# Kernel optimization log

Measured on AMD Instinct MI355X. Metric: run time of the kernel, lower is better.

## Reference

```python
import jax, jax.numpy as jnp
import numpy as np

KERNEL_MUL = 2.0
KERNEL_NUM = 5


def setup_inputs() -> dict:
    key = jax.random.key(0)
    k1, k2 = jax.random.split(key)
    source_features = jax.random.normal(k1, (4096, 1024), dtype=jnp.float32)
    target_features = jax.random.normal(k2, (4096, 1024), dtype=jnp.float32)
    return {"source_features": source_features, "target_features": target_features}


def reference(source_features, target_features):
    n = source_features.shape[0]
    total = jnp.concatenate([source_features, target_features], axis=0)  # [L, D]
    L = total.shape[0]
    # Pairwise squared distances via gram trick (same math as sum((a-b)**2)).
    sq = jnp.sum(total * total, axis=1)  # [L]
    d2 = jnp.maximum(sq[:, None] + sq[None, :] - 2.0 * (total @ total.T), 0.0)  # [L, L]
    # Median-heuristic-style bandwidth: mean of off-diagonal distances.
    bandwidth = jnp.sum(d2) / (L * L - L)
    bandwidth = bandwidth / (KERNEL_MUL ** (KERNEL_NUM // 2))
    # Multi-bandwidth RBF kernel sum (fixed small loop over KERNEL_NUM).
    kernel = jnp.zeros_like(d2)
    for i in range(KERNEL_NUM):
        kernel = kernel + jnp.exp(-d2 / (bandwidth * (KERNEL_MUL ** i)))
    kernel = kernel / KERNEL_NUM
    ss = jnp.mean(kernel[:n, :n])
    tt = jnp.mean(kernel[n:, n:])
    st = jnp.mean(kernel[:n, n:])
    return ss + tt - 2.0 * st
```

## Files before the change

kernel.cpp:

```cpp
#include <hip/hip_runtime.h>
#include <hip/hip_bf16.h>
#include <stdint.h>


#define L_TOTAL 8192
#define D_FEAT  1024
#define N_HALF  4096
#define TILE    128
#define TTILES  64
#define NBLK    (TTILES*(TTILES+1)/2)
#define BK      64

typedef __bf16 bf16_t;
typedef __bf16 bf16x4_t __attribute__((ext_vector_type(4)));
typedef __bf16 bf16x8_t __attribute__((ext_vector_type(8)));
typedef float  f32x4_t  __attribute__((ext_vector_type(4)));

#define XB_OFF   0
#define SQ_OFF   (L_TOTAL * D_FEAT * 2)
#define COL_OFF  (SQ_OFF + L_TOTAL * 4)
#define SACC_OFF (COL_OFF + D_FEAT * 4)
#define C1_OFF   (SACC_OFF + 8)

__device__ __forceinline__ void async_ld16(void* lds, const void* g) {
  auto ldsp = (__attribute__((address_space(3))) void*)(uintptr_t)lds;
  auto gp   = (const __attribute__((address_space(1))) void*)(uintptr_t)g;
  __builtin_amdgcn_global_load_lds(gp, ldsp, 16, 0, 0);
}

extern "C" __global__ __launch_bounds__(256) void k_zero(
    float* __restrict__ colsum, double* __restrict__ S_acc)
{
  const int tid = threadIdx.x;
  for (int c = tid; c < D_FEAT; c += 256) colsum[c] = 0.f;
  if (tid == 0) *S_acc = 0.0;
}

extern "C" __global__ __launch_bounds__(256) void k_prep(
    const float* __restrict__ src, const float* __restrict__ tgt,
    bf16_t* __restrict__ Xb, float* __restrict__ sq, float* __restrict__ colsum)
{
  __shared__ float cs[4][D_FEAT];
  const int tid  = threadIdx.x;
  const int lane = tid & 63;
  const int w    = tid >> 6;
  const int rbase = blockIdx.x * 32 + w * 8;

  float csp[16];
  #pragma unroll
  for (int j = 0; j < 16; ++j) csp[j] = 0.f;

  for (int i = 0; i < 8; ++i) {
    const int row = rbase + i;
    const float* xr = (row < N_HALF) ? (src + (size_t)row * D_FEAT)
                                     : (tgt + (size_t)(row - N_HALF) * D_FEAT);
    float s = 0.f;
    #pragma unroll
    for (int q = 0; q < 4; ++q) {
      const float4 v = ((const float4*)xr)[q * 64 + lane];
      bf16x4_t bv;
      bv[0] = (bf16_t)v.x; bv[1] = (bf16_t)v.y; bv[2] = (bf16_t)v.z; bv[3] = (bf16_t)v.w;
      *(bf16x4_t*)(Xb + (size_t)row * D_FEAT + (q * 64 + lane) * 4) = bv;
      const float g0 = (float)bv[0], g1 = (float)bv[1], g2 = (float)bv[2], g3 = (float)bv[3];
      s += g0 * g0 + g1 * g1 + g2 * g2 + g3 * g3;
      csp[q * 4 + 0] += v.x; csp[q * 4 + 1] += v.y;
      csp[q * 4 + 2] += v.z; csp[q * 4 + 3] += v.w;
    }
    #pragma unroll
    for (int off = 32; off > 0; off >>= 1) s += __shfl_down(s, off);
    if (lane == 0) sq[row] = s;
  }

  #pragma unroll
  for (int q = 0; q < 4; ++q) {
    float4 v4 = make_float4(csp[q*4+0], csp[q*4+1], csp[q*4+2], csp[q*4+3]);
    *(float4*)&cs[w][(q * 64 + lane) * 4] = v4;
  }
  __syncthreads();
  #pragma unroll
  for (int k = 0; k < 4; ++k) {
    const int c = tid * 4 + k;
    atomicAdd(&colsum[c], cs[0][c] + cs[1][c] + cs[2][c] + cs[3][c]);
  }
}

extern "C" __global__ __launch_bounds__(1024) void k_bw(
    const float* __restrict__ sq, const float* __restrict__ colsum,
    float* __restrict__ c1out)
{
  const int tid = threadIdx.x;
  double t = 0.0;
  for (int i = tid; i < L_TOTAL; i += 1024) t += (double)sq[i];
  t *= 2.0 * (double)L_TOTAL;
  if (tid < D_FEAT) { double v = colsum[tid]; t -= 2.0 * v * v; }
  __shared__ double red[1024];
  red[tid] = t;
  __syncthreads();
  for (int off = 512; off > 0; off >>= 1) {
    if (tid < off) red[tid] += red[tid + off];
    __syncthreads();
  }
  if (tid == 0) {
    double bw = red[0] / ((double)L_TOTAL * (double)L_TOTAL - (double)L_TOTAL);
    bw = bw / 4.0;
    *c1out = (float)(-1.4426950408889634 / (16.0 * bw));
  }
}

extern "C" __global__ __launch_bounds__(256) void k_mmd(
    const bf16_t* __restrict__ Xb, const float* __restrict__ sq,
    const float* __restrict__ c1ptr, double* __restrict__ S_acc)
{
  __shared__ __align__(16) char smem[2 * TILE * BK * 2];
  bf16_t* As = (bf16_t*)smem;
  bf16_t* Bs = (bf16_t*)(smem + TILE * BK * 2);

  const int b = (blockIdx.x & 7) * (NBLK / 8) + (blockIdx.x >> 3);
  int ti = (int)((sqrtf(8.f * (float)b + 1.f) - 1.f) * 0.5f);
  while ((ti + 1) * (ti + 2) / 2 <= b) ++ti;
  while (ti * (ti + 1) / 2 > b) --ti;
  const int tj = b - ti * (ti + 1) / 2;
  const int row0 = ti * TILE, col0 = tj * TILE;

  const int tid  = threadIdx.x;
  const int lane = tid & 63;
  const int w    = tid >> 6;
  const int wr   = w >> 1, wc = w & 1;

  const int srow = lane >> 3;
  const int scol = ((lane & 7) ^ srow) * 8;
  uint32_t offA[4], offB[4];
  #pragma unroll
  for (int q = 0; q < 4; ++q) {
    const int ch = w * 4 + q;
    offA[q] = (uint32_t)(row0 + ch * 8 + srow) * D_FEAT + scol;
    offB[q] = (uint32_t)(col0 + ch * 8 + srow) * D_FEAT + scol;
  }

  const int x = lane >> 4, y = lane & 7, rlo = lane & 15;
  const int baA0 = (wr * 64 + rlo) * (BK * 2) + ((x ^ y) * 16);
  const int baB0 = (wc * 64 + rlo) * (BK * 2) + ((x ^ y) * 16);
  const int baA1 = baA0 ^ 64;
  const int baB1 = baB0 ^ 64;
  const char* Ac = (const char*)As;
  const char* Bc = (const char*)Bs;

  f32x4_t acc[4][4] = {};

  for (int k0 = 0; k0 < D_FEAT; k0 += BK) {
    #pragma unroll
    for (int q = 0; q < 4; ++q) {
      async_ld16(&As[(w * 4 + q) * 512], Xb + offA[q] + k0);
      async_ld16(&Bs[(w * 4 + q) * 512], Xb + offB[q] + k0);
    }
    __syncthreads();

    bf16x8_t af0[4], af1[4], bf0[4], bf1[4];
    #pragma unroll
    for (int m = 0; m < 4; ++m) {
      af0[m] = *(const bf16x8_t*)(Ac + baA0 + m * 2048);
      af1[m] = *(const bf16x8_t*)(Ac + baA1 + m * 2048);
    }
    #pragma unroll
    for (int n = 0; n < 4; ++n) {
      bf0[n] = *(const bf16x8_t*)(Bc + baB0 + n * 2048);
      bf1[n] = *(const bf16x8_t*)(Bc + baB1 + n * 2048);
    }
    #pragma unroll
    for (int m = 0; m < 4; ++m)
      #pragma unroll
      for (int n = 0; n < 4; ++n)
        acc[m][n] = __builtin_amdgcn_mfma_f32_16x16x32_bf16(af0[m], bf0[n], acc[m][n], 0, 0, 0);
    #pragma unroll
    for (int m = 0; m < 4; ++m)
      #pragma unroll
      for (int n = 0; n < 4; ++n)
        acc[m][n] = __builtin_amdgcn_mfma_f32_16x16x32_bf16(af1[m], bf1[n], acc[m][n], 0, 0, 0);
    __syncthreads();
  }

  const float c1   = *c1ptr;
  const float sgn  = ((ti < TTILES / 2) == (tj < TTILES / 2)) ? 1.f : -1.f;
  const float wgt  = (ti == tj ? 1.f : 2.f) * sgn;
  float part = 0.f;
  const int colb = col0 + wc * 64 + rlo;
  const int rowb = row0 + wr * 64 + x * 4;
  #pragma unroll
  for (int m = 0; m < 4; ++m) {
    #pragma unroll
    for (int n = 0; n < 4; ++n) {
      const float sqj = sq[colb + n * 16];
      #pragma unroll
      for (int r = 0; r < 4; ++r) {
        const float sqi = sq[rowb + m * 16 + r];
        float d2 = fmaxf(sqi + sqj - 2.f * acc[m][n][r], 0.f);
        const float e  = __builtin_amdgcn_exp2f(d2 * c1);
        const float e2 = e * e, e4 = e2 * e2, e8 = e4 * e4, e16 = e8 * e8;
        part += e + e2 + e4 + e8 + e16;
      }
    }
  }
  part *= wgt;

  #pragma unroll
  for (int off = 32; off > 0; off >>= 1) part += __shfl_down(part, off);
  float* red = (float*)smem;
  __syncthreads();
  if (lane == 0) red[w] = part;
  __syncthreads();
  if (tid == 0)
    atomicAdd(S_acc, (double)(red[0] + red[1] + red[2] + red[3]));
}

extern "C" __global__ void k_fin(const double* __restrict__ S_acc, float* __restrict__ out)
{
  out[0] = (float)(*S_acc / (5.0 * (double)N_HALF * (double)N_HALF));
}

extern "C" void kernel_launch(void* const* d_in, const int* in_sizes, int n_in,
                              void* d_out, int out_size, void* d_ws, size_t ws_size,
                              hipStream_t stream) {
  const float* src = (const float*)d_in[0];
  const float* tgt = (const float*)d_in[1];
  float* out = (float*)d_out;
  char* ws = (char*)d_ws;
  bf16_t* Xb     = (bf16_t*)(ws + XB_OFF);
  float*  sq     = (float*)(ws + SQ_OFF);
  float*  colsum = (float*)(ws + COL_OFF);
  double* S_acc  = (double*)(ws + SACC_OFF);
  float*  c1     = (float*)(ws + C1_OFF);

  k_zero<<<1, 256, 0, stream>>>(colsum, S_acc);
  k_prep<<<256, 256, 0, stream>>>(src, tgt, Xb, sq, colsum);
  k_bw  <<<1, 1024, 0, stream>>>(sq, colsum, c1);
  k_mmd <<<NBLK, 256, 0, stream>>>(Xb, sq, c1, S_acc);
  k_fin <<<1, 1, 0, stream>>>(S_acc, out);
}
```

Baseline: 221.6 us.

## Halve GEMM K-tile, replicate column-sum atomics, and memset accumulators

The main GEMM loop now uses a K-tile of 32 instead of 64, which halves LDS use per block to raise occupancy, with a new swizzle for the narrower rows. The price is twice as many barriers per block. The prep kernel uses twice as many blocks, each covering half the rows. Its column-sum atomics are spread over 16 replicated buffers to cut contention, and the bandwidth kernel sums the replicas. The zero-init kernel is replaced by a hipMemsetAsync over the accumulator region.

Result: faster. 189.8 us (-14.4%).

```diff
diff --git a/kernel.cpp b/kernel.cpp
--- a/kernel.cpp
+++ b/kernel.cpp
@@ -9,7 +9,8 @@
 #define TILE    128
 #define TTILES  64
 #define NBLK    (TTILES*(TTILES+1)/2)
-#define BK      64
+#define BK      32
+#define REPL    16
 
 typedef __bf16 bf16_t;
 typedef __bf16 bf16x4_t __attribute__((ext_vector_type(4)));
@@ -18,9 +19,11 @@
 
 #define XB_OFF   0
 #define SQ_OFF   (L_TOTAL * D_FEAT * 2)
-#define COL_OFF  (SQ_OFF + L_TOTAL * 4)
-#define SACC_OFF (COL_OFF + D_FEAT * 4)
-#define C1_OFF   (SACC_OFF + 8)
+#define MS_OFF   (SQ_OFF + L_TOTAL * 4)
+#define SACC_OFF (MS_OFF)
+#define COL_OFF  (MS_OFF + 8)
+#define MS_BYTES (8 + REPL * D_FEAT * 4)
+#define C1_OFF   (MS_OFF + MS_BYTES)
 
 __device__ __forceinline__ void async_ld16(void* lds, const void* g) {
   auto ldsp = (__attribute__((address_space(3))) void*)(uintptr_t)lds;
@@ -28,14 +31,6 @@
   __builtin_amdgcn_global_load_lds(gp, ldsp, 16, 0, 0);
 }
 
-extern "C" __global__ __launch_bounds__(256) void k_zero(
-    float* __restrict__ colsum, double* __restrict__ S_acc)
-{
-  const int tid = threadIdx.x;
-  for (int c = tid; c < D_FEAT; c += 256) colsum[c] = 0.f;
-  if (tid == 0) *S_acc = 0.0;
-}
-
 extern "C" __global__ __launch_bounds__(256) void k_prep(
     const float* __restrict__ src, const float* __restrict__ tgt,
     bf16_t* __restrict__ Xb, float* __restrict__ sq, float* __restrict__ colsum)
@@ -44,13 +39,14 @@
   const int tid  = threadIdx.x;
   const int lane = tid & 63;
   const int w    = tid >> 6;
-  const int rbase = blockIdx.x * 32 + w * 8;
+  const int rbase = blockIdx.x * 16 + w * 4;
 
   float csp[16];
   #pragma unroll
   for (int j = 0; j < 16; ++j) csp[j] = 0.f;
 
-  for (int i = 0; i < 8; ++i) {
+  #pragma unroll
+  for (int i = 0; i < 4; ++i) {
     const int row = rbase + i;
     const float* xr = (row < N_HALF) ? (src + (size_t)row * D_FEAT)
                                      : (tgt + (size_t)(row - N_HALF) * D_FEAT);
@@ -77,10 +73,11 @@
     *(float4*)&cs[w][(q * 64 + lane) * 4] = v4;
   }
   __syncthreads();
+  float* crep = colsum + (blockIdx.x & (REPL - 1)) * D_FEAT;
   #pragma unroll
   for (int k = 0; k < 4; ++k) {
     const int c = tid * 4 + k;
-    atomicAdd(&colsum[c], cs[0][c] + cs[1][c] + cs[2][c] + cs[3][c]);
+    atomicAdd(&crep[c], cs[0][c] + cs[1][c] + cs[2][c] + cs[3][c]);
   }
 }
 
@@ -92,7 +89,12 @@
   double t = 0.0;
   for (int i = tid; i < L_TOTAL; i += 1024) t += (double)sq[i];
   t *= 2.0 * (double)L_TOTAL;
-  if (tid < D_FEAT) { double v = colsum[tid]; t -= 2.0 * v * v; }
+  if (tid < D_FEAT) {
+    float csum = 0.f;
+    #pragma unroll
+    for (int r = 0; r < REPL; ++r) csum += colsum[r * D_FEAT + tid];
+    t -= 2.0 * (double)csum * (double)csum;
+  }
   __shared__ double red[1024];
   red[tid] = t;
   __syncthreads();
@@ -111,9 +113,8 @@
     const bf16_t* __restrict__ Xb, const float* __restrict__ sq,
     const float* __restrict__ c1ptr, double* __restrict__ S_acc)
 {
-  __shared__ __align__(16) char smem[2 * TILE * BK * 2];
-  bf16_t* As = (bf16_t*)smem;
-  bf16_t* Bs = (bf16_t*)(smem + TILE * BK * 2);
+  __shared__ __align__(16) bf16_t As[TILE * BK];
+  __shared__ __align__(16) bf16_t Bs[TILE * BK];
 
   const int b = (blockIdx.x & 7) * (NBLK / 8) + (blockIdx.x >> 3);
   int ti = (int)((sqrtf(8.f * (float)b + 1.f) - 1.f) * 0.5f);
@@ -127,55 +128,44 @@
   const int w    = tid >> 6;
   const int wr   = w >> 1, wc = w & 1;
 
-  const int srow = lane >> 3;
-  const int scol = ((lane & 7) ^ srow) * 8;
-  uint32_t offA[4], offB[4];
-  #pragma unroll
-  for (int q = 0; q < 4; ++q) {
-    const int ch = w * 4 + q;
-    offA[q] = (uint32_t)(row0 + ch * 8 + srow) * D_FEAT + scol;
-    offB[q] = (uint32_t)(col0 + ch * 8 + srow) * D_FEAT + scol;
-  }
-
-  const int x = lane >> 4, y = lane & 7, rlo = lane & 15;
-  const int baA0 = (wr * 64 + rlo) * (BK * 2) + ((x ^ y) * 16);
-  const int baB0 = (wc * 64 + rlo) * (BK * 2) + ((x ^ y) * 16);
-  const int baA1 = baA0 ^ 64;
-  const int baB1 = baB0 ^ 64;
+  f32x4_t acc[4][4] = {};
+
+  const int srow = lane >> 2;
+  const int scol = (((lane & 3) - (lane >> 3)) & 3) * 8;
+  uint32_t offA[2], offB[2];
+  #pragma unroll
+  for (int q = 0; q < 2; ++q) {
+    const int ch = w * 2 + q;
+    offA[q] = (uint32_t)(row0 + ch * 16 + srow) * D_FEAT + scol;
+    offB[q] = (uint32_t)(col0 + ch * 16 + srow) * D_FEAT + scol;
+  }
+
+  const int rlo = lane & 15, x = lane >> 4;
+  const int p   = (x + (rlo >> 1)) & 3;
+  const int baA = (wr * 64 + rlo) * (BK * 2) + p * 16;
+  const int baB = (wc * 64 + rlo) * (BK * 2) + p * 16;
   const char* Ac = (const char*)As;
   const char* Bc = (const char*)Bs;
 
-  f32x4_t acc[4][4] = {};
-
   for (int k0 = 0; k0 < D_FEAT; k0 += BK) {
     #pragma unroll
-    for (int q = 0; q < 4; ++q) {
-      async_ld16(&As[(w * 4 + q) * 512], Xb + offA[q] + k0);
-      async_ld16(&Bs[(w * 4 + q) * 512], Xb + offB[q] + k0);
+    for (int q = 0; q < 2; ++q) {
+      async_ld16(&As[(w * 2 + q) * 512], Xb + offA[q] + k0);
+      async_ld16(&Bs[(w * 2 + q) * 512], Xb + offB[q] + k0);
     }
     __syncthreads();
 
-    bf16x8_t af0[4], af1[4], bf0[4], bf1[4];
-    #pragma unroll
-    for (int m = 0; m < 4; ++m) {
-      af0[m] = *(const bf16x8_t*)(Ac + baA0 + m * 2048);
-      af1[m] = *(const bf16x8_t*)(Ac + baA1 + m * 2048);
-    }
-    #pragma unroll
-    for (int n = 0; n < 4; ++n) {
-      bf0[n] = *(const bf16x8_t*)(Bc + baB0 + n * 2048);
-      bf1[n] = *(const bf16x8_t*)(Bc + baB1 + n * 2048);
-    }
+    bf16x8_t af[4], bfr[4];
+    #pragma unroll
+    for (int m = 0; m < 4; ++m) af[m]  = *(const bf16x8_t*)(Ac + baA + m * 1024);
+    #pragma unroll
+    for (int n = 0; n < 4; ++n) bfr[n] = *(const bf16x8_t*)(Bc + baB + n * 1024);
+
     #pragma unroll
     for (int m = 0; m < 4; ++m)
       #pragma unroll
       for (int n = 0; n < 4; ++n)
-        acc[m][n] = __builtin_amdgcn_mfma_f32_16x16x32_bf16(af0[m], bf0[n], acc[m][n], 0, 0, 0);
-    #pragma unroll
-    for (int m = 0; m < 4; ++m)
-      #pragma unroll
-      for (int n = 0; n < 4; ++n)
-        acc[m][n] = __builtin_amdgcn_mfma_f32_16x16x32_bf16(af1[m], bf1[n], acc[m][n], 0, 0, 0);
+        acc[m][n] = __builtin_amdgcn_mfma_f32_16x16x32_bf16(af[m], bfr[n], acc[m][n], 0, 0, 0);
     __syncthreads();
   }
 
@@ -204,7 +194,7 @@
 
   #pragma unroll
   for (int off = 32; off > 0; off >>= 1) part += __shfl_down(part, off);
-  float* red = (float*)smem;
+  float* red = (float*)As;
   __syncthreads();
   if (lane == 0) red[w] = part;
   __syncthreads();
@@ -226,12 +216,12 @@
   char* ws = (char*)d_ws;
   bf16_t* Xb     = (bf16_t*)(ws + XB_OFF);
   float*  sq     = (float*)(ws + SQ_OFF);
+  double* S_acc  = (double*)(ws + SACC_OFF);
   float*  colsum = (float*)(ws + COL_OFF);
-  double* S_acc  = (double*)(ws + SACC_OFF);
   float*  c1     = (float*)(ws + C1_OFF);
 
-  k_zero<<<1, 256, 0, stream>>>(colsum, S_acc);
-  k_prep<<<256, 256, 0, stream>>>(src, tgt, Xb, sq, colsum);
+  hipMemsetAsync(ws + MS_OFF, 0, MS_BYTES, stream);
+  k_prep<<<512, 256, 0, stream>>>(src, tgt, Xb, sq, colsum);
   k_bw  <<<1, 1024, 0, stream>>>(sq, colsum, c1);
   k_mmd <<<NBLK, 256, 0, stream>>>(Xb, sq, c1, S_acc);
   k_fin <<<1, 1, 0, stream>>>(S_acc, out);
```
